# Kernel tuning notes

Measured on AMD Instinct MI355X. Metric: run time of the kernel, lower is better.

The kernel has to match this reference:

```python
import jax, jax.numpy as jnp
import numpy as np

B, C, LO, LQ, H = 64, 4, 64, 128, 768
NEG = -10000.0


def _trilinear(u, um, v, vm, w1, b1, w2, b2, w3):
    # u: [N, Lu, H], v: [N, Lv, H]; returns [N, Lu, Lv]
    p1 = u @ w1 + b1                                  # [N, Lu, 1]
    p2 = (v @ w2 + b2).transpose(0, 2, 1)             # [N, 1, Lv]
    p3 = jnp.einsum('bud,bvd->buv', u * w3, v)        # trilinear term
    return p1 + p2 + p3 + ((1.0 - um) * NEG)[:, :, None] + ((1.0 - vm) * NEG)[:, None, :]


def _forward(encoded_o, encoded_q, om, qm,
             att_W1_w, att_W1_b, att_W2_w, att_W2_b, att_W3,
             Wc_self_w, Wc_self_b, Wc_w, Wc_b, Va_w, Va_b, Wg_w, Wg_b,
             co_W1_w, co_W1_b, co_W2_w, co_W2_b, co_W3, Wp_w, Wp_b,
             sa_W1_w, sa_W1_b, sa_W2_w, sa_W2_b, sa_W3, Wf_w, Wf_b):
    b, c, lo, h = encoded_o.shape
    lq = encoded_q.shape[2]
    p = c * (c - 1)
    # ---- pairwise option-compare (OCN_Att_layer) over all (i, j), j != i ----
    i_idx = np.repeat(np.arange(c), c - 1)
    j_idx = np.array([j for i in range(c) for j in range(c) if j != i])
    o_i = encoded_o[:, i_idx].reshape(b * p, lo, h)   # 'ok'
    o_j = encoded_o[:, j_idx].reshape(b * p, lo, h)   # 'ol'
    m_i = om[:, i_idx].reshape(b * p, lo)
    m_j = om[:, j_idx].reshape(b * p, lo)
    A = _trilinear(o_j, m_j, o_i, m_i, att_W1_w, att_W1_b, att_W2_w, att_W2_b, att_W3)
    att = jax.nn.softmax(A, axis=1)
    olk_ctx = jnp.einsum('bud,buv->bvd', o_j, att)    # [BP, LO, H]
    OLK = jnp.concatenate([o_i - olk_ctx, o_i * olk_ctx], axis=-1)  # [BP, LO, 2H]
    cmp_proj = OLK @ Wc_w + Wc_b                      # Wc applied per compare pair
    cmp_sum = cmp_proj.reshape(b, c, c - 1, lo, h).sum(axis=2).reshape(b * c, lo, h)
    # ---- merge layer (per candidate, flattened into batch) ----
    o1 = encoded_o.reshape(b * c, lo, h)
    q = encoded_q.reshape(b * c, lq, h)
    omf = om.reshape(b * c, lo)
    qmf = qm.reshape(b * c, lq)
    Aq = jax.nn.softmax(q @ Va_w + Va_b + ((1.0 - qmf) * NEG)[:, :, None], axis=1)  # [BC, LQ, 1]
    Q = jnp.einsum('bld,blo->bod', q, Aq)             # [BC, 1, H]
    OCK = jnp.tanh(o1 @ Wc_self_w + Wc_self_b + cmp_sum)
    Qb = jnp.broadcast_to(Q, (b * c, lo, h))
    G = jax.nn.sigmoid(jnp.concatenate([o1, OCK, Qb], axis=-1) @ Wg_w + Wg_b)
    merged = G * o1 + (1.0 - G) * OCK                 # [BC, LO, H]
    # ---- co-attention with question ----
    A2 = _trilinear(q, qmf, merged, omf, co_W1_w, co_W1_b, co_W2_w, co_W2_b, co_W3)  # [BC, LQ, LO]
    ACK = jax.nn.softmax(A2, axis=2)
    OA = jnp.einsum('bqo,bod->bqd', ACK, merged)      # [BC, LQ, H]
    APK = jax.nn.softmax(A2, axis=1)
    dOA = jnp.concatenate([q, OA], axis=-1)           # [BC, LQ, 2H]
    POAA = jnp.einsum('bqd,bqo->bod', dOA, APK)       # [BC, LO, 2H]
    OPK = jax.nn.relu(jnp.concatenate([merged, POAA], axis=-1) @ Wp_w + Wp_b)
    # ---- self-attention ----
    A3 = _trilinear(OPK, omf, OPK, omf, sa_W1_w, sa_W1_b, sa_W2_w, sa_W2_b, sa_W3)
    att3 = jax.nn.softmax(A3, axis=1)
    OSK = jnp.einsum('bud,buv->bvd', OPK, att3)
    OFK = jax.nn.relu(jnp.concatenate([OPK, OSK, OPK - OSK, OPK * OSK], axis=-1) @ Wf_w + Wf_b)
    return OFK.reshape(b, c, lo, h).max(axis=2)       # [B, C, H]


def setup_inputs():
    ks = jax.random.split(jax.random.key(0), 32)
    def p(i, shape, s=0.02):
        return jax.random.normal(ks[i], shape, jnp.float32) * s
    return {
        'encoded_o': jax.random.normal(ks[0], (B, C, LO, H), jnp.float32),
        'encoded_q': jax.random.normal(ks[1], (B, C, LQ, H), jnp.float32),
        'option_mask': jnp.ones((B, C, LO), jnp.int32),
        'question_mask': jnp.ones((B, C, LQ), jnp.int32),
        'att_W1_w': p(2, (H, 1)), 'att_W1_b': p(3, (1,)),
        'att_W2_w': p(4, (H, 1)), 'att_W2_b': p(5, (1,)),
        'att_W3': p(6, (H,)),
        'Wc_self_w': p(7, (H, H)), 'Wc_self_b': p(8, (H,)),
        'Wc_w': p(9, (2 * H, H)), 'Wc_b': p(10, (H,)),
        'Va_w': p(11, (H, 1)), 'Va_b': p(12, (1,)),
        'Wg_w': p(13, (3 * H, H)), 'Wg_b': p(14, (H,)),
        'co_W1_w': p(15, (H, 1)), 'co_W1_b': p(16, (1,)),
        'co_W2_w': p(17, (H, 1)), 'co_W2_b': p(18, (1,)),
        'co_W3': p(19, (H,)),
        'Wp_w': p(20, (3 * H, H)), 'Wp_b': p(21, (H,)),
        'sa_W1_w': p(22, (H, 1)), 'sa_W1_b': p(23, (1,)),
        'sa_W2_w': p(24, (H, 1)), 'sa_W2_b': p(25, (1,)),
        'sa_W3': p(26, (H,)),
        'Wf_w': p(27, (4 * H, H)), 'Wf_b': p(28, (H,)),
    }


def reference(encoded_o, encoded_q, option_mask, question_mask,
              att_W1_w, att_W1_b, att_W2_w, att_W2_b, att_W3,
              Wc_self_w, Wc_self_b, Wc_w, Wc_b, Va_w, Va_b, Wg_w, Wg_b,
              co_W1_w, co_W1_b, co_W2_w, co_W2_b, co_W3, Wp_w, Wp_b,
              sa_W1_w, sa_W1_b, sa_W2_w, sa_W2_b, sa_W3, Wf_w, Wf_b):
    return _forward(encoded_o, encoded_q,
                    option_mask.astype(jnp.float32), question_mask.astype(jnp.float32),
                    att_W1_w, att_W1_b, att_W2_w, att_W2_b, att_W3,
                    Wc_self_w, Wc_self_b, Wc_w, Wc_b, Va_w, Va_b, Wg_w, Wg_b,
                    co_W1_w, co_W1_b, co_W2_w, co_W2_b, co_W3, Wp_w, Wp_b,
                    sa_W1_w, sa_W1_b, sa_W2_w, sa_W2_b, sa_W3, Wf_w, Wf_b)
```

## Files before the change

kernel.cpp:

```cpp
#include <hip/hip_runtime.h>
#include <math.h>


#define NEGC (-10000.0f)
constexpr int HD = 768;
constexpr int KSTR = 9216;

constexpr int EP_TANH = 1;
constexpr int EP_MERGE = 2;
constexpr int EP_RELU = 3;
constexpr int EP_RELU_MAX = 4;

typedef __attribute__((ext_vector_type(8))) short bf16x8;
typedef __attribute__((ext_vector_type(8))) unsigned short u16x8;
typedef __attribute__((ext_vector_type(4))) unsigned short u16x4;
typedef __attribute__((ext_vector_type(4))) float f32x4;

__device__ inline void st8(float* dst, float4 a0, float4 a1) {
  dst[0] = a0.x; dst[1] = a0.y; dst[2] = a0.z; dst[3] = a0.w;
  dst[4] = a1.x; dst[5] = a1.y; dst[6] = a1.z; dst[7] = a1.w;
}

__device__ inline unsigned short f2bf(float x) {
  unsigned int u = __float_as_uint(x);
  u += 0x7fffu + ((u >> 16) & 1u);
  return (unsigned short)(u >> 16);
}

__device__ inline float bf2f(unsigned short u) {
  return __uint_as_float(((unsigned int)u) << 16);
}

__device__ inline u16x8 pack8(float4 a, float4 b) {
  u16x8 r;
  r[0] = f2bf(a.x); r[1] = f2bf(a.y); r[2] = f2bf(a.z); r[3] = f2bf(a.w);
  r[4] = f2bf(b.x); r[5] = f2bf(b.y); r[6] = f2bf(b.z); r[7] = f2bf(b.w);
  return r;
}

__device__ inline u16x4 pack4(float4 a) {
  u16x4 r;
  r[0] = f2bf(a.x); r[1] = f2bf(a.y); r[2] = f2bf(a.z); r[3] = f2bf(a.w);
  return r;
}

__device__ inline void gload_lds16(const unsigned short* src, unsigned short* dst) {
  __builtin_amdgcn_global_load_lds(
      (const __attribute__((address_space(1))) void*)src,
      (__attribute__((address_space(3))) void*)dst, 16, 0, 0);
}

__global__ __launch_bounds__(256)
void bfprep_dot_kernel(const float* __restrict__ x, const float* __restrict__ w3,
                       const float* __restrict__ w1, const float* __restrict__ b1,
                       const float* __restrict__ w2, const float* __restrict__ b2,
                       unsigned short* __restrict__ xbf, unsigned short* __restrict__ xw3,
                       float* __restrict__ o1, float* __restrict__ o2, int ntok) {
  int tok = blockIdx.x * 4 + (threadIdx.x >> 6);
  int lane = threadIdx.x & 63;
  if (tok >= ntok) return;
  const float* xp = x + (size_t)tok * HD;
  unsigned short* xb = xbf + (size_t)tok * HD;
  unsigned short* xw = xw3 + (size_t)tok * HD;
  float s1 = 0.f, s2 = 0.f;
#pragma unroll
  for (int i = 0; i < 3; ++i) {
    int c = (lane + (i << 6)) << 2;
    float4 xv = *(const float4*)(xp + c);
    float4 w3v = *(const float4*)(w3 + c);
    float4 wa = *(const float4*)(w1 + c);
    float4 wb = *(const float4*)(w2 + c);
    s1 = fmaf(xv.x, wa.x, s1); s1 = fmaf(xv.y, wa.y, s1);
    s1 = fmaf(xv.z, wa.z, s1); s1 = fmaf(xv.w, wa.w, s1);
    s2 = fmaf(xv.x, wb.x, s2); s2 = fmaf(xv.y, wb.y, s2);
    s2 = fmaf(xv.z, wb.z, s2); s2 = fmaf(xv.w, wb.w, s2);
    *(u16x4*)(xb + c) = pack4(xv);
    float4 sv;
    sv.x = xv.x * w3v.x; sv.y = xv.y * w3v.y; sv.z = xv.z * w3v.z; sv.w = xv.w * w3v.w;
    *(u16x4*)(xw + c) = pack4(sv);
  }
#pragma unroll
  for (int off = 32; off; off >>= 1) {
    s1 += __shfl_xor(s1, off);
    s2 += __shfl_xor(s2, off);
  }
  if (lane == 0) { o1[tok] = s1 + b1[0]; o2[tok] = s2 + b2[0]; }
}

__global__ __launch_bounds__(256)
void opkprep_kernel(const unsigned short* __restrict__ x, const float* __restrict__ w3,
                    const float* __restrict__ w1, const float* __restrict__ b1,
                    const float* __restrict__ w2, const float* __restrict__ b2,
                    unsigned short* __restrict__ xw3,
                    float* __restrict__ o1, float* __restrict__ o2, int ntok) {
  int tok = blockIdx.x * 4 + (threadIdx.x >> 6);
  int lane = threadIdx.x & 63;
  if (tok >= ntok) return;
  const unsigned short* xp = x + (size_t)tok * HD;
  unsigned short* xw = xw3 + (size_t)tok * HD;
  float s1 = 0.f, s2 = 0.f;
#pragma unroll
  for (int i = 0; i < 3; ++i) {
    int c = (lane + (i << 6)) << 2;
    u16x4 xv = *(const u16x4*)(xp + c);
    float x0 = bf2f(xv[0]), x1 = bf2f(xv[1]), x2 = bf2f(xv[2]), x3 = bf2f(xv[3]);
    float4 w3v = *(const float4*)(w3 + c);
    float4 wa = *(const float4*)(w1 + c);
    float4 wb = *(const float4*)(w2 + c);
    s1 = fmaf(x0, wa.x, s1); s1 = fmaf(x1, wa.y, s1);
    s1 = fmaf(x2, wa.z, s1); s1 = fmaf(x3, wa.w, s1);
    s2 = fmaf(x0, wb.x, s2); s2 = fmaf(x1, wb.y, s2);
    s2 = fmaf(x2, wb.z, s2); s2 = fmaf(x3, wb.w, s2);
    u16x4 sv;
    sv[0] = f2bf(x0 * w3v.x); sv[1] = f2bf(x1 * w3v.y);
    sv[2] = f2bf(x2 * w3v.z); sv[3] = f2bf(x3 * w3v.w);
    *(u16x4*)(xw + c) = sv;
  }
#pragma unroll
  for (int off = 32; off; off >>= 1) {
    s1 += __shfl_xor(s1, off);
    s2 += __shfl_xor(s2, off);
  }
  if (lane == 0) { o1[tok] = s1 + b1[0]; o2[tok] = s2 + b2[0]; }
}

__global__ __launch_bounds__(256)
void qpool2_kernel(const float* __restrict__ q,
                   const float* __restrict__ Va_w, const float* __restrict__ Va_b,
                   const float* __restrict__ coW1_w, const float* __restrict__ coW1_b,
                   const int* __restrict__ qm,
                   float* __restrict__ qco1, float* __restrict__ Q) {
  __shared__ float qa_s[128];
  __shared__ float wgt[128];
  __shared__ float wred[4];
  const int t = threadIdx.x, bc = blockIdx.x;
  const int lane = t & 63, wv = t >> 6;
  const float* qb = q + (size_t)bc * (128 * HD);
  for (int it = 0; it < 32; ++it) {
    const int tl = it * 4 + wv;
    const float* xp = qb + (size_t)tl * HD;
    float s1 = 0.f, s2 = 0.f;
#pragma unroll
    for (int i = 0; i < 3; ++i) {
      int c = (lane + (i << 6)) << 2;
      float4 xv = *(const float4*)(xp + c);
      float4 wa = *(const float4*)(Va_w + c);
      float4 wb = *(const float4*)(coW1_w + c);
      s1 = fmaf(xv.x, wa.x, s1); s1 = fmaf(xv.y, wa.y, s1);
      s1 = fmaf(xv.z, wa.z, s1); s1 = fmaf(xv.w, wa.w, s1);
      s2 = fmaf(xv.x, wb.x, s2); s2 = fmaf(xv.y, wb.y, s2);
      s2 = fmaf(xv.z, wb.z, s2); s2 = fmaf(xv.w, wb.w, s2);
    }
#pragma unroll
    for (int off = 32; off; off >>= 1) {
      s1 += __shfl_xor(s1, off);
      s2 += __shfl_xor(s2, off);
    }
    if (lane == 0) {
      qa_s[tl] = s1 + Va_b[0];
      qco1[bc * 128 + tl] = s2 + coW1_b[0];
    }
  }
  __syncthreads();
  const int* qmp = qm + bc * 128;
  float v = -1e30f;
  if (t < 128) v = qa_s[t] + (1.f - (float)qmp[t]) * NEGC;
  float m = v;
#pragma unroll
  for (int off = 32; off; off >>= 1) m = fmaxf(m, __shfl_xor(m, off));
  if ((t & 63) == 0) wred[t >> 6] = m;
  __syncthreads();
  float gm = fmaxf(fmaxf(wred[0], wred[1]), fmaxf(wred[2], wred[3]));
  float e = (t < 128) ? expf(v - gm) : 0.f;
  float s = e;
#pragma unroll
  for (int off = 32; off; off >>= 1) s += __shfl_xor(s, off);
  __syncthreads();
  if ((t & 63) == 0) wred[t >> 6] = s;
  __syncthreads();
  float tot = wred[0] + wred[1] + wred[2] + wred[3];
  if (t < 128) wgt[t] = e / tot;
  __syncthreads();
  float* Qp = Q + (size_t)bc * HD;
  for (int d = t; d < HD; d += 256) {
    float acc = 0.f;
    for (int l = 0; l < 128; ++l) acc = fmaf(wgt[l], qb[(size_t)l * HD + d], acc);
    Qp[d] = acc;
  }
}

template<int NJ>
__global__ __launch_bounds__(256)
void p1_kernel(const unsigned short* __restrict__ Xbf, const unsigned short* __restrict__ Xw3,
               const float* __restrict__ s1g, const float* __restrict__ s2g,
               const int* __restrict__ maskg, unsigned short* __restrict__ PtG) {
  __shared__ __align__(16) unsigned short Ua[64 * 136];
  __shared__ __align__(16) unsigned short Vb[64 * 136];
  __shared__ float Sbuf[64][66];
  __shared__ float red[4][64];
  const int t = threadIdx.x;
  int ubc, vbc;
  if (NJ == 1) {
    ubc = vbc = blockIdx.x;
  } else {
    const int b = blockIdx.x / 12, pr = blockIdx.x % 12;
    const int i = pr / 3, jj = pr % 3;
    const int j = jj + (jj >= i ? 1 : 0);
    vbc = (b << 2) + i; ubc = (b << 2) + j;
  }
  const unsigned short* U = Xbf + (size_t)ubc * (64 * HD);
  const unsigned short* V = Xw3 + (size_t)vbc * (64 * HD);
  const int w = t >> 6, lane = t & 63, l15 = lane & 15, l4 = lane >> 4;
  const int srow = t >> 2, scol = (t & 3) << 5;
  f32x4 acc[4] = {};
  for (int k0 = 0; k0 < HD; k0 += 128) {
    const unsigned short* up = U + (size_t)srow * HD + k0 + scol;
    const unsigned short* vp = V + (size_t)srow * HD + k0 + scol;
    unsigned short* ua = &Ua[srow * 136 + scol];
    unsigned short* vb = &Vb[srow * 136 + scol];
#pragma unroll
    for (int z = 0; z < 4; ++z) {
      *(u16x8*)(ua + z * 8) = *(const u16x8*)(up + z * 8);
      *(u16x8*)(vb + z * 8) = *(const u16x8*)(vp + z * 8);
    }
    __syncthreads();
#pragma unroll
    for (int ks = 0; ks < 4; ++ks) {
      bf16x8 af = *(const bf16x8*)(&Ua[(w * 16 + l15) * 136 + ks * 32 + l4 * 8]);
#pragma unroll
      for (int n = 0; n < 4; ++n) {
        bf16x8 bf = *(const bf16x8*)(&Vb[(n * 16 + l15) * 136 + ks * 32 + l4 * 8]);
        acc[n] = __builtin_amdgcn_mfma_f32_16x16x32_bf16(af, bf, acc[n], 0, 0, 0);
      }
    }
    __syncthreads();
  }
  {
    float s1v[4];
#pragma unroll
    for (int r = 0; r < 4; ++r) {
      int u = w * 16 + l4 * 4 + r;
      s1v[r] = s1g[ubc * 64 + u] + (1.f - (float)maskg[ubc * 64 + u]) * NEGC;
    }
#pragma unroll
    for (int n = 0; n < 4; ++n) {
      int v = n * 16 + l15;
      float s2v = s2g[vbc * 64 + v] + (1.f - (float)maskg[vbc * 64 + v]) * NEGC;
#pragma unroll
      for (int r = 0; r < 4; ++r)
        Sbuf[w * 16 + l4 * 4 + r][v] = acc[n][r] + s1v[r] + s2v;
    }
  }
  __syncthreads();
  {
    const int v = t & 63, part = t >> 6;
    float m = -1e30f;
#pragma unroll
    for (int z = 0; z < 16; ++z) m = fmaxf(m, Sbuf[part * 16 + z][v]);
    red[part][v] = m;
    __syncthreads();
    float gm = fmaxf(fmaxf(red[0][v], red[1][v]), fmaxf(red[2][v], red[3][v]));
    float s = 0.f;
#pragma unroll
    for (int z = 0; z < 16; ++z) {
      float e = expf(Sbuf[part * 16 + z][v] - gm);
      Sbuf[part * 16 + z][v] = e;
      s += e;
    }
    __syncthreads();
    red[part][v] = s;
    __syncthreads();
    float cinv = 1.f / (red[0][v] + red[1][v] + red[2][v] + red[3][v]);
    unsigned short* pt = PtG + (size_t)blockIdx.x * 4096 + v * 64 + part * 16;
#pragma unroll
    for (int z = 0; z < 16; ++z) pt[z] = f2bf(Sbuf[part * 16 + z][v] * cinv);
  }
}

template<int NJ>
__global__ __launch_bounds__(256)
void p2_kernel(const unsigned short* __restrict__ Xbf, const unsigned short* __restrict__ PtG,
               const unsigned short* __restrict__ Oi,
               unsigned short* __restrict__ osk,
               unsigned short* __restrict__ y1, unsigned short* __restrict__ y2) {
  __shared__ __align__(16) unsigned short Pts[NJ][64 * 72];
  __shared__ __align__(16) unsigned short U2[64 * 192];
  const int t = threadIdx.x;
  const int dq = blockIdx.x, bc = blockIdx.y;
  const int d0 = dq * 192;
  const int b = bc >> 2, i = bc & 3;
  const int w = t >> 6, lane = t & 63, l15 = lane & 15, l4 = lane >> 4;
  {
    const int v = t >> 2, cs = (t & 3) << 4;
#pragma unroll
    for (int jj = 0; jj < NJ; ++jj) {
      size_t src = (NJ == 1 ? (size_t)bc : (size_t)(b * 12 + i * 3 + jj)) * 4096 + v * 64 + cs;
      *(u16x8*)(&Pts[jj][v * 72 + cs]) = *(const u16x8*)(PtG + src);
      *(u16x8*)(&Pts[jj][v * 72 + cs + 8]) = *(const u16x8*)(PtG + src + 8);
    }
  }
  f32x4 acc[4][3] = {};
  const int su = t >> 2, sc0 = (t & 3) * 48;
  const int sswz = ((su >> 3) & 3) << 5;
  for (int jj = 0; jj < NJ; ++jj) {
    const int ubc = (NJ == 1) ? bc : ((b << 2) + (jj + (jj >= i ? 1 : 0)));
    __syncthreads();
    {
      const unsigned short* up = Xbf + (size_t)ubc * (64 * HD) + (size_t)su * HD + d0 + sc0;
#pragma unroll
      for (int it = 0; it < 6; ++it) {
        u16x8 vdat = *(const u16x8*)(up + it * 8);
        *(u16x8*)((char*)U2 + ((su * 384 + (sc0 + it * 8) * 2) ^ sswz)) = vdat;
      }
    }
    __syncthreads();
    const unsigned short* ptj = &Pts[jj][0];
#pragma unroll
    for (int ks = 0; ks < 2; ++ks) {
      bf16x8 bfr[3];
#pragma unroll
      for (int n = 0; n < 3; ++n) {
        const int col = (w * 3 + n) * 16 + l15;
#pragma unroll
        for (int e = 0; e < 8; ++e) {
          const int uk = ks * 32 + l4 * 8 + e;
          const int byte = (uk * 384 + col * 2) ^ (((uk >> 3) & 3) << 5);
          bfr[n][e] = *(const short*)((const char*)U2 + byte);
        }
      }
#pragma unroll
      for (int m = 0; m < 4; ++m) {
        bf16x8 af = *(const bf16x8*)(ptj + (m * 16 + l15) * 72 + ks * 32 + l4 * 8);
#pragma unroll
        for (int n = 0; n < 3; ++n)
          acc[m][n] = __builtin_amdgcn_mfma_f32_16x16x32_bf16(af, bfr[n], acc[m][n], 0, 0, 0);
      }
    }
  }
  const unsigned short* oip = Oi + (size_t)bc * (64 * HD);
  const size_t obase = (size_t)bc * (64 * HD);
#pragma unroll
  for (int m = 0; m < 4; ++m)
#pragma unroll
    for (int n = 0; n < 3; ++n) {
      const int d = d0 + (w * 3 + n) * 16 + l15;
#pragma unroll
      for (int r = 0; r < 4; ++r) {
        const int v = m * 16 + l4 * 4 + r;
        const size_t idx = obase + (size_t)v * HD + d;
        const float cs = acc[m][n][r];
        const float oi = bf2f(oip[(size_t)v * HD + d]);
        if (NJ == 3) {
          y1[idx] = f2bf(fmaf(3.f, oi, -cs));
          y2[idx] = f2bf(oi * cs);
        } else {
          osk[idx] = f2bf(cs);
          y1[idx] = f2bf(oi - cs);
          y2[idx] = f2bf(oi * cs);
        }
      }
    }
}

__global__ __launch_bounds__(256)
void poaa2_kernel(const float* __restrict__ qin, const unsigned short* __restrict__ mergedb,
                  const float* __restrict__ qco1,
                  const float* __restrict__ coW2_w, const float* __restrict__ coW2_b,
                  const int* __restrict__ qm, const int* __restrict__ om,
                  const float* __restrict__ w3,
                  unsigned short* __restrict__ PLO, unsigned short* __restrict__ PHI) {
  __shared__ __align__(16) char smem[77312];
  __shared__ float red[4][64];
  __shared__ float rowm[128], rowfac[128];
  __shared__ float colfac[64];
  __shared__ float ms2_s[64];
  __shared__ float gmax_s;
  float* T = (float*)smem;
  unsigned short* Aq = (unsigned short*)smem;
  unsigned short* Bm = (unsigned short*)(smem + 18432);
  unsigned short* Tt = (unsigned short*)(smem + 33280);
  unsigned short* Tft = (unsigned short*)(smem + 50688);
  unsigned short* M2bf = (unsigned short*)(smem + 68096);
  unsigned short* Qc = (unsigned short*)smem;
  unsigned short* Mc = (unsigned short*)(smem + 18432);

  const int t = threadIdx.x, dqh = blockIdx.x, bc = blockIdx.y;
  const int w = t >> 6, lane = t & 63, l15 = lane & 15, l4 = lane >> 4;
  const float* qp = qin + (size_t)bc * (128 * HD);
  const unsigned short* mp = mergedb + (size_t)bc * (64 * HD);
  const float* qc = qco1 + bc * 128;
  const int* qmp = qm + bc * 128;
  const int* omp = om + bc * 64;

  {
    const int arow = t >> 1, acs = (t & 1) << 5;
    const int brow = t >> 2, bcs = (t & 3) << 4;
    f32x4 acc[2][4] = {};
    float msacc = 0.f;
    for (int k0 = 0; k0 < HD; k0 += 64) {
      {
        const float* p = qp + (size_t)arow * HD + k0 + acs;
        const float* wp = w3 + k0 + acs;
        unsigned short* dst = &Aq[arow * 72 + acs];
#pragma unroll
        for (int z = 0; z < 4; ++z) {
          float4 a = *(const float4*)(p + z * 8);
          float4 b = *(const float4*)(p + z * 8 + 4);
          float4 wa = *(const float4*)(wp + z * 8);
          float4 wb = *(const float4*)(wp + z * 8 + 4);
          a.x *= wa.x; a.y *= wa.y; a.z *= wa.z; a.w *= wa.w;
          b.x *= wb.x; b.y *= wb.y; b.z *= wb.z; b.w *= wb.w;
          *(u16x8*)(dst + z * 8) = pack8(a, b);
        }
      }
      {
        const unsigned short* p = mp + (size_t)brow * HD + k0 + bcs;
        unsigned short* dst = &Bm[brow * 72 + bcs];
        u16x8 v0 = *(const u16x8*)(p);
        u16x8 v1 = *(const u16x8*)(p + 8);
        *(u16x8*)(dst) = v0;
        *(u16x8*)(dst + 8) = v1;
        const float* wp = coW2_w + k0 + bcs;
        float4 wa = *(const float4*)(wp);
        float4 wb = *(const float4*)(wp + 4);
        float4 wc = *(const float4*)(wp + 8);
        float4 wd = *(const float4*)(wp + 12);
        msacc = fmaf(bf2f(v0[0]), wa.x, msacc); msacc = fmaf(bf2f(v0[1]), wa.y, msacc);
        msacc = fmaf(bf2f(v0[2]), wa.z, msacc); msacc = fmaf(bf2f(v0[3]), wa.w, msacc);
        msacc = fmaf(bf2f(v0[4]), wb.x, msacc); msacc = fmaf(bf2f(v0[5]), wb.y, msacc);
        msacc = fmaf(bf2f(v0[6]), wb.z, msacc); msacc = fmaf(bf2f(v0[7]), wb.w, msacc);
        msacc = fmaf(bf2f(v1[0]), wc.x, msacc); msacc = fmaf(bf2f(v1[1]), wc.y, msacc);
        msacc = fmaf(bf2f(v1[2]), wc.z, msacc); msacc = fmaf(bf2f(v1[3]), wc.w, msacc);
        msacc = fmaf(bf2f(v1[4]), wd.x, msacc); msacc = fmaf(bf2f(v1[5]), wd.y, msacc);
        msacc = fmaf(bf2f(v1[6]), wd.z, msacc); msacc = fmaf(bf2f(v1[7]), wd.w, msacc);
      }
      __syncthreads();
#pragma unroll
      for (int ks = 0; ks < 2; ++ks) {
        bf16x8 af[2], bf[4];
#pragma unroll
        for (int m = 0; m < 2; ++m)
          af[m] = *(const bf16x8*)(&Aq[(w * 32 + m * 16 + l15) * 72 + ks * 32 + l4 * 8]);
#pragma unroll
        for (int n = 0; n < 4; ++n)
          bf[n] = *(const bf16x8*)(&Bm[(n * 16 + l15) * 72 + ks * 32 + l4 * 8]);
#pragma unroll
        for (int m = 0; m < 2; ++m)
#pragma unroll
          for (int n = 0; n < 4; ++n)
            acc[m][n] = __builtin_amdgcn_mfma_f32_16x16x32_bf16(af[m], bf[n], acc[m][n], 0, 0, 0);
      }
      __syncthreads();
    }
    msacc += __shfl_xor(msacc, 1);
    msacc += __shfl_xor(msacc, 2);
    if ((t & 3) == 0) ms2_s[brow] = msacc + coW2_b[0];
    __syncthreads();
#pragma unroll
    for (int n = 0; n < 4; ++n) {
      const int v = n * 16 + l15;
      const float ct = ms2_s[v] + (1.f - (float)omp[v]) * NEGC;
#pragma unroll
      for (int m = 0; m < 2; ++m)
#pragma unroll
        for (int r = 0; r < 4; ++r) {
          const int qrow = w * 32 + m * 16 + l4 * 4 + r;
          const float rt = qc[qrow] + (1.f - (float)qmp[qrow]) * NEGC;
          T[qrow * 65 + v] = acc[m][n][r] + rt + ct;
        }
    }
  }
  __syncthreads();
  {
    int qrow = t >> 1, h = t & 1;
    float m = -1e30f;
    for (int v = h * 32; v < h * 32 + 32; ++v) m = fmaxf(m, T[qrow * 65 + v]);
    m = fmaxf(m, __shfl_xor(m, 1));
    float s = 0.f;
    for (int v = h * 32; v < h * 32 + 32; ++v) s += expf(T[qrow * 65 + v] - m);
    s += __shfl_xor(s, 1);
    if (h == 0) { rowm[qrow] = m; rowfac[qrow] = s; }
  }
  float colm_loc = 0.f;
  {
    int v = t & 63, part = t >> 6;
    float m = -1e30f;
    for (int qq = part * 32; qq < part * 32 + 32; ++qq) m = fmaxf(m, T[qq * 65 + v]);
    red[part][v] = m;
    __syncthreads();
    float cm = fmaxf(fmaxf(red[0][v], red[1][v]), fmaxf(red[2][v], red[3][v]));
    float s = 0.f;
    for (int qq = part * 32; qq < part * 32 + 32; ++qq) s += expf(T[qq * 65 + v] - cm);
    __syncthreads();
    red[part][v] = s;
    __syncthreads();
    if (part == 0) { colm_loc = cm; colfac[v] = red[0][v] + red[1][v] + red[2][v] + red[3][v]; }
  }
  __syncthreads();
  if (t < 64) {
    float m = fmaxf(rowm[t], rowm[t + 64]);
#pragma unroll
    for (int off = 32; off; off >>= 1) m = fmaxf(m, __shfl_xor(m, off));
    if (t == 0) gmax_s = m;
  }
  __syncthreads();
  const float gmax = gmax_s;
  if (t < 128) rowfac[t] = expf(fminf(gmax - rowm[t], 60.f)) / rowfac[t];
  if (t < 64) colfac[t] = expf(fminf(gmax - colm_loc, 60.f)) / colfac[t];
  __syncthreads();
  {
    const int o = t >> 2, qs = (t & 3) << 5;
    for (int z = 0; z < 32; ++z) {
      const int qq = qs + z;
      float e = expf(T[qq * 65 + o] - gmax);
      Tt[o * 136 + qq] = f2bf(e);
      Tft[o * 136 + qq] = f2bf(e * rowfac[qq]);
    }
  }
  __syncthreads();
  {
    f32x4 m2acc[4] = {};
#pragma unroll
    for (int ks = 0; ks < 4; ++ks) {
      bf16x8 af = *(const bf16x8*)(&Tt[(w * 16 + l15) * 136 + ks * 32 + l4 * 8]);
#pragma unroll
      for (int n = 0; n < 4; ++n) {
        bf16x8 bf = *(const bf16x8*)(&Tft[(n * 16 + l15) * 136 + ks * 32 + l4 * 8]);
        m2acc[n] = __builtin_amdgcn_mfma_f32_16x16x32_bf16(af, bf, m2acc[n], 0, 0, 0);
      }
    }
#pragma unroll
    for (int n = 0; n < 4; ++n)
#pragma unroll
      for (int r = 0; r < 4; ++r) {
        const int o = w * 16 + l4 * 4 + r;
        M2bf[o * 72 + n * 16 + l15] = f2bf(colfac[o] * m2acc[n][r]);
      }
  }
  const int dql = t >> 1, dqs = (t & 1) << 5;
  const int dml = t >> 2, dms = (t & 3) << 4;
  const int swq = ((dql >> 3) & 3) << 5;
  const int swm = ((dml >> 3) & 3) << 5;
  unsigned short* plo = PLO + (size_t)bc * (64 * HD);
  unsigned short* phi = PHI + (size_t)bc * (64 * HD);
  for (int dc = dqh * 6; dc < dqh * 6 + 6; ++dc) {
    const int d0 = dc * 64;
    __syncthreads();
    {
      const float* p = qp + (size_t)dql * HD + d0 + dqs;
#pragma unroll
      for (int z = 0; z < 4; ++z) {
        float4 a = *(const float4*)(p + z * 8);
        float4 b = *(const float4*)(p + z * 8 + 4);
        *(u16x8*)((char*)Qc + ((dql * 144 + (dqs + z * 8) * 2) ^ swq)) = pack8(a, b);
      }
    }
    {
      const unsigned short* p = mp + (size_t)dml * HD + d0 + dms;
      *(u16x8*)((char*)Mc + ((dml * 144 + dms * 2) ^ swm)) = *(const u16x8*)p;
      *(u16x8*)((char*)Mc + ((dml * 144 + (dms + 8) * 2) ^ swm)) = *(const u16x8*)(p + 8);
    }
    __syncthreads();
    const int col = w * 16 + l15;
    f32x4 lacc[4] = {};
#pragma unroll
    for (int ks = 0; ks < 4; ++ks) {
      bf16x8 bf;
#pragma unroll
      for (int e = 0; e < 8; ++e) {
        const int qq = ks * 32 + l4 * 8 + e;
        bf[e] = *(const short*)((const char*)Qc + ((qq * 144 + col * 2) ^ (((qq >> 3) & 3) << 5)));
      }
#pragma unroll
      for (int m = 0; m < 4; ++m) {
        bf16x8 af = *(const bf16x8*)(&Tt[(m * 16 + l15) * 136 + ks * 32 + l4 * 8]);
        lacc[m] = __builtin_amdgcn_mfma_f32_16x16x32_bf16(af, bf, lacc[m], 0, 0, 0);
      }
    }
    f32x4 pacc[4] = {};
#pragma unroll
    for (int ks = 0; ks < 2; ++ks) {
      bf16x8 bf;
#pragma unroll
      for (int e = 0; e < 8; ++e) {
        const int vv = ks * 32 + l4 * 8 + e;
        bf[e] = *(const short*)((const char*)Mc + ((vv * 144 + col * 2) ^ (((vv >> 3) & 3) << 5)));
      }
#pragma unroll
      for (int m = 0; m < 4; ++m) {
        bf16x8 af = *(const bf16x8*)(&M2bf[(m * 16 + l15) * 72 + ks * 32 + l4 * 8]);
        pacc[m] = __builtin_amdgcn_mfma_f32_16x16x32_bf16(af, bf, pacc[m], 0, 0, 0);
      }
    }
#pragma unroll
    for (int m = 0; m < 4; ++m)
#pragma unroll
      for (int r = 0; r < 4; ++r) {
        const int o = m * 16 + l4 * 4 + r;
        const int d = d0 + w * 16 + l15;
        plo[(size_t)o * HD + d] = f2bf(colfac[o] * lacc[m][r]);
        phi[(size_t)o * HD + d] = f2bf(pacc[m][r]);
      }
  }
}

struct GemmArgs {
  const float* a[4];
  const float* w[4];
  int nchunks;
  const float* bias;
  float* out;
};

__global__ __launch_bounds__(256)
void gemm_store_kernel(GemmArgs g) {
  __shared__ float As[64][33];
  __shared__ float Ws[32][65];
  const int t = threadIdx.x;
  const int m0 = blockIdx.y << 6, n0 = blockIdx.x << 6;
  const int tr = t >> 4, tc = t & 15;
  float acc[4][4];
#pragma unroll
  for (int x = 0; x < 4; ++x)
#pragma unroll
    for (int y = 0; y < 4; ++y) acc[x][y] = 0.f;
  const int arow = t >> 2, acs = (t & 3) << 3;
  const int wrow = t >> 3, wcs = (t & 7) << 3;
  for (int c = 0; c < g.nchunks; ++c) {
    const float* Ap = g.a[c] + (size_t)(m0 + arow) * HD + acs;
    const float* Wp = g.w[c] + (size_t)wrow * HD + n0 + wcs;
    for (int k0 = 0; k0 < HD; k0 += 32) {
      float4 a0 = *(const float4*)(Ap + k0);
      float4 a1 = *(const float4*)(Ap + k0 + 4);
      st8(&As[arow][acs], a0, a1);
      float4 w0 = *(const float4*)(Wp + (size_t)k0 * HD);
      float4 w1 = *(const float4*)(Wp + (size_t)k0 * HD + 4);
      st8(&Ws[wrow][wcs], w0, w1);
      __syncthreads();
#pragma unroll
      for (int kk = 0; kk < 32; ++kk) {
        float av[4], bv[4];
#pragma unroll
        for (int x = 0; x < 4; ++x) av[x] = As[(tr << 2) + x][kk];
#pragma unroll
        for (int y = 0; y < 4; ++y) bv[y] = Ws[kk][(tc << 2) + y];
#pragma unroll
        for (int x = 0; x < 4; ++x)
#pragma unroll
          for (int y = 0; y < 4; ++y) acc[x][y] = fmaf(av[x], bv[y], acc[x][y]);
      }
      __syncthreads();
    }
  }
#pragma unroll
  for (int x = 0; x < 4; ++x) {
    const int r = m0 + (tr << 2) + x;
#pragma unroll
    for (int y = 0; y < 4; ++y) {
      const int n = n0 + (tc << 2) + y;
      g.out[(size_t)r * HD + n] = acc[x][y] + g.bias[n];
    }
  }
}

struct WcAllArgs {
  const float* src[12];
  int basecol[12];
  unsigned short* dst;
};

__global__ __launch_bounds__(256)
void wconv_all_kernel(WcAllArgs g) {
  __shared__ float tile[64][65];
  const int slice = blockIdx.y;
  const float* src = g.src[slice];
  const int bi = blockIdx.x % 12, bj = blockIdx.x / 12;
  const int t = threadIdx.x;
  const int r = t >> 2, cseg = (t & 3) << 4;
  const float* p = src + (size_t)(bi * 64 + r) * HD + bj * 64 + cseg;
#pragma unroll
  for (int j = 0; j < 16; j += 4) {
    float4 v = *(const float4*)(p + j);
    tile[r][cseg + j + 0] = v.x; tile[r][cseg + j + 1] = v.y;
    tile[r][cseg + j + 2] = v.z; tile[r][cseg + j + 3] = v.w;
  }
  __syncthreads();
  unsigned short* q = g.dst + (size_t)(bj * 64 + r) * KSTR + g.basecol[slice] + bi * 64 + cseg;
  u16x8 lo, hi;
#pragma unroll
  for (int j = 0; j < 8; ++j) lo[j] = f2bf(tile[cseg + j][r]);
#pragma unroll
  for (int j = 0; j < 8; ++j) hi[j] = f2bf(tile[cseg + 8 + j][r]);
  *(u16x8*)q = lo;
  *(u16x8*)(q + 8) = hi;
}

struct MMArgs {
  const unsigned short* a[4];
  int K;
  const unsigned short* wt;
  const float* bias;
  const float* bias2;
  const unsigned short* aux0;
  const unsigned short* aux1;
  const float* aux2;
  float* outf;
  unsigned short* outb;
};

template<int EP>
__global__ __launch_bounds__(512)
void mfma_gemm_kernel(MMArgs g) {
  __shared__ __align__(16) unsigned short As[3][128 * 32];
  __shared__ __align__(16) unsigned short Bs[3][128 * 32];
  const int t = threadIdx.x;
  const int lane = t & 63, w = t >> 6;
  const int wr = w >> 2, wc = w & 3;
  const int m0 = blockIdx.x << 7, n0 = blockIdx.y << 7;
  const int l15 = lane & 15, l4 = lane >> 4;
  f32x4 acc[4][2] = {};

  const int srow = w * 16 + (lane >> 2);
  const int gcol = (((lane & 3) ^ ((lane >> 3) & 3))) * 8;
  const int rsw = (l15 >> 1) & 3;
  const int rcol = ((l4 ^ rsw)) * 8;

  const int nkt = g.K >> 5;

  auto issue = [&](int kt, int buf) {
    const int c = kt / 24;
    const int koff = (kt - c * 24) << 5;
    const unsigned short* ap = g.a[c] + (size_t)(m0 + srow) * HD + koff + gcol;
    const unsigned short* bp = g.wt + (size_t)(n0 + srow) * KSTR + (kt << 5) + gcol;
    gload_lds16(ap, &As[buf][w * 512]);
    gload_lds16(bp, &Bs[buf][w * 512]);
  };

  auto compute = [&](int kt, int buf, bool prefetch) {
    bf16x8 af[4], bfr[2];
#pragma unroll
    for (int mi = 0; mi < 4; ++mi)
      af[mi] = *(const bf16x8*)(&As[buf][(wr * 64 + mi * 16 + l15) * 32 + rcol]);
#pragma unroll
    for (int ni = 0; ni < 2; ++ni)
      bfr[ni] = *(const bf16x8*)(&Bs[buf][(wc * 32 + ni * 16 + l15) * 32 + rcol]);
    asm volatile("s_waitcnt lgkmcnt(0)" ::: "memory");
    __builtin_amdgcn_s_barrier();
    if (prefetch) issue(kt + 3, buf);
    __builtin_amdgcn_s_setprio(1);
#pragma unroll
    for (int mi = 0; mi < 4; ++mi)
#pragma unroll
      for (int ni = 0; ni < 2; ++ni)
        acc[mi][ni] = __builtin_amdgcn_mfma_f32_16x16x32_bf16(af[mi], bfr[ni], acc[mi][ni], 0, 0, 0);
    __builtin_amdgcn_s_setprio(0);
  };

  issue(0, 0); issue(1, 1); issue(2, 2);
  int buf = 0;
  int kt = 0;
  for (; kt < nkt - 2; ++kt) {
    asm volatile("s_waitcnt vmcnt(4)" ::: "memory");
    __builtin_amdgcn_s_barrier();
    compute(kt, buf, kt + 3 < nkt);
    buf = (buf == 2) ? 0 : buf + 1;
  }
  asm volatile("s_waitcnt vmcnt(2)" ::: "memory");
  __builtin_amdgcn_s_barrier();
  compute(kt, buf, false);
  buf = (buf == 2) ? 0 : buf + 1;
  ++kt;
  asm volatile("s_waitcnt vmcnt(0)" ::: "memory");
  __builtin_amdgcn_s_barrier();
  compute(kt, buf, false);

  if (EP == EP_RELU_MAX) {
#pragma unroll
    for (int ni = 0; ni < 2; ++ni) {
      const int n = n0 + wc * 32 + ni * 16 + l15;
      const float b = g.bias[n];
      float m = 0.f;
#pragma unroll
      for (int mi = 0; mi < 4; ++mi)
#pragma unroll
        for (int r = 0; r < 4; ++r)
          m = fmaxf(m, acc[mi][ni][r] + b);
      m = fmaxf(m, 0.f);
      m = fmaxf(m, __shfl_xor(m, 16));
      m = fmaxf(m, __shfl_xor(m, 32));
      if (l4 == 0) g.outf[(size_t)((m0 >> 6) + wr) * HD + n] = m;
    }
  } else {
#pragma unroll
    for (int mi = 0; mi < 4; ++mi)
#pragma unroll
      for (int r = 0; r < 4; ++r) {
        const int row = m0 + wr * 64 + mi * 16 + l4 * 4 + r;
#pragma unroll
        for (int ni = 0; ni < 2; ++ni) {
          const int n = n0 + wc * 32 + ni * 16 + l15;
          const size_t oi = (size_t)row * HD + n;
          float v = acc[mi][ni][r];
          if (EP == EP_TANH) {
            g.outb[oi] = f2bf(tanhf(v + g.bias[n] + 3.f * g.bias2[n]));
          } else if (EP == EP_MERGE) {
            float gg = v + g.aux2[(size_t)(row >> 6) * HD + n];
            float sg = 1.f / (1.f + expf(-gg));
            float o1v = bf2f(g.aux0[oi]);
            float ock = bf2f(g.aux1[oi]);
            g.outb[oi] = f2bf(fmaf(sg, o1v - ock, ock));
          } else {
            g.outb[oi] = f2bf(fmaxf(v + g.bias[n], 0.f));
          }
        }
      }
  }
}

extern "C" void kernel_launch(void* const* d_in, const int* in_sizes, int n_in,
                              void* d_out, int out_size, void* d_ws, size_t ws_size,
                              hipStream_t stream) {
  const float* enc_o = (const float*)d_in[0];
  const float* enc_q = (const float*)d_in[1];
  const int* om = (const int*)d_in[2];
  const int* qm = (const int*)d_in[3];
  const float* att_W1_w = (const float*)d_in[4];
  const float* att_W1_b = (const float*)d_in[5];
  const float* att_W2_w = (const float*)d_in[6];
  const float* att_W2_b = (const float*)d_in[7];
  const float* att_W3 = (const float*)d_in[8];
  const float* Wc_self_w = (const float*)d_in[9];
  const float* Wc_self_b = (const float*)d_in[10];
  const float* Wc_w = (const float*)d_in[11];
  const float* Wc_b = (const float*)d_in[12];
  const float* Va_w = (const float*)d_in[13];
  const float* Va_b = (const float*)d_in[14];
  const float* Wg_w = (const float*)d_in[15];
  const float* Wg_b = (const float*)d_in[16];
  const float* co_W1_w = (const float*)d_in[17];
  const float* co_W1_b = (const float*)d_in[18];
  const float* co_W2_w = (const float*)d_in[19];
  const float* co_W2_b = (const float*)d_in[20];
  const float* co_W3 = (const float*)d_in[21];
  const float* Wp_w = (const float*)d_in[22];
  const float* Wp_b = (const float*)d_in[23];
  const float* sa_W1_w = (const float*)d_in[24];
  const float* sa_W1_b = (const float*)d_in[25];
  const float* sa_W2_w = (const float*)d_in[26];
  const float* sa_W2_b = (const float*)d_in[27];
  const float* sa_W3 = (const float*)d_in[28];
  const float* Wf_w = (const float*)d_in[29];
  const float* Wf_b = (const float*)d_in[30];
  float* out = (float*)d_out;

  const int NTOK_O = 16384;
  const int HH = 768 * 768;

  float* ws = (float*)d_ws;
  size_t off = 0;
  auto carve = [&](size_t n) { float* p = ws + off; off += n; return p; };
  float* s1o   = carve(16384);
  float* s2o   = carve(16384);
  float* qco1  = carve(32768);
  float* sa1   = carve(16384);
  float* sa2   = carve(16384);
  float* Qpool = carve(196608);
  float* Qg    = carve(196608);
  float* A2buf = carve(2097152);
  float* r1 = carve(12582912);
  float* r2 = carve(12582912);
  float* r3 = carve(12582912);
  float* r4 = carve(12582912);
  if (ws_size < off * sizeof(float)) return;
  unsigned short* OPKb  = (unsigned short*)r1;
  unsigned short* X1    = (unsigned short*)(r1 + 6291456);
  unsigned short* X3    = (unsigned short*)(r1 + 6291456);
  unsigned short* OCKb  = (unsigned short*)r2;
  unsigned short* PLOb  = (unsigned short*)r2;
  unsigned short* opkw3 = (unsigned short*)r2;
  unsigned short* X2    = (unsigned short*)(r2 + 6291456);
  unsigned short* MRGb  = (unsigned short*)r3;
  unsigned short* OSKb  = (unsigned short*)r3;
  unsigned short* X4    = (unsigned short*)(r3 + 6291456);
  unsigned short* eobf  = (unsigned short*)r4;
  unsigned short* eow3  = (unsigned short*)(r4 + 6291456);
  unsigned short* PHIb  = (unsigned short*)r4;
  unsigned short* wall  = (unsigned short*)(r4 + 6291456);
  unsigned short* PtG   = (unsigned short*)A2buf;

  const dim3 GBIG(128, 6);

  bfprep_dot_kernel<<<NTOK_O / 4, 256, 0, stream>>>(enc_o, att_W3, att_W1_w, att_W1_b,
                                                    att_W2_w, att_W2_b, eobf, eow3,
                                                    s1o, s2o, NTOK_O);
  qpool2_kernel<<<256, 256, 0, stream>>>(enc_q, Va_w, Va_b, co_W1_w, co_W1_b,
                                         qm, qco1, Qpool);

  p1_kernel<3><<<768, 256, 0, stream>>>(eobf, eow3, s1o, s2o, om, PtG);
  {
    WcAllArgs wa{};
    wa.src[0] = Wc_self_w; wa.src[1] = Wc_w;        wa.src[2] = Wc_w + HH;
    wa.src[3] = Wg_w;      wa.src[4] = Wg_w + HH;
    wa.src[5] = Wp_w;      wa.src[6] = Wp_w + HH;   wa.src[7] = Wp_w + 2 * HH;
    wa.src[8] = Wf_w;      wa.src[9] = Wf_w + HH;   wa.src[10] = Wf_w + 2 * HH;
    wa.src[11] = Wf_w + 3 * HH;
    int bases[12] = {0, 768, 1536, 2304, 3072, 3840, 4608, 5376, 6144, 6912, 7680, 8448};
    for (int i = 0; i < 12; ++i) wa.basecol[i] = bases[i];
    wa.dst = wall;
    wconv_all_kernel<<<dim3(144, 12), 256, 0, stream>>>(wa);
  }
  p2_kernel<3><<<dim3(4, 256), 256, 0, stream>>>(eobf, PtG, eobf, nullptr, X1, X2);

  {
    MMArgs g{};
    g.a[0] = eobf; g.a[1] = X1; g.a[2] = X2;
    g.K = 2304; g.wt = wall + 0;
    g.bias = Wc_self_b; g.bias2 = Wc_b; g.outb = OCKb;
    mfma_gemm_kernel<EP_TANH><<<GBIG, 512, 0, stream>>>(g);
  }

  {
    GemmArgs g{};
    g.a[0] = Qpool; g.w[0] = Wg_w + 2 * HH;
    g.nchunks = 1; g.bias = Wg_b; g.out = Qg;
    gemm_store_kernel<<<dim3(12, 4), 256, 0, stream>>>(g);
  }

  {
    MMArgs g{};
    g.a[0] = eobf; g.a[1] = OCKb;
    g.K = 1536; g.wt = wall + 2304; g.bias = nullptr;
    g.aux0 = eobf; g.aux1 = OCKb; g.aux2 = Qg; g.outb = MRGb;
    mfma_gemm_kernel<EP_MERGE><<<GBIG, 512, 0, stream>>>(g);
  }

  poaa2_kernel<<<dim3(2, 256), 256, 0, stream>>>(enc_q, MRGb, qco1, co_W2_w, co_W2_b,
                                                 qm, om, co_W3, PLOb, PHIb);

  {
    MMArgs g{};
    g.a[0] = MRGb; g.a[1] = PLOb; g.a[2] = PHIb;
    g.K = 2304; g.wt = wall + 3840; g.bias = Wp_b; g.outb = OPKb;
    mfma_gemm_kernel<EP_RELU><<<GBIG, 512, 0, stream>>>(g);
  }

  opkprep_kernel<<<NTOK_O / 4, 256, 0, stream>>>(OPKb, sa_W3, sa_W1_w, sa_W1_b,
                                                 sa_W2_w, sa_W2_b, opkw3, sa1, sa2, NTOK_O);
  p1_kernel<1><<<256, 256, 0, stream>>>(OPKb, opkw3, sa1, sa2, om, PtG);
  p2_kernel<1><<<dim3(4, 256), 256, 0, stream>>>(OPKb, PtG, OPKb, OSKb, X3, X4);

  {
    MMArgs g{};
    g.a[0] = OPKb; g.a[1] = OSKb; g.a[2] = X3; g.a[3] = X4;
    g.K = 3072; g.wt = wall + 6144; g.bias = Wf_b; g.outf = out;
    mfma_gemm_kernel<EP_RELU_MAX><<<GBIG, 512, 0, stream>>>(g);
  }
}
```

Baseline: 599.6 us.

## Widen GEMM K-tile to 64 with double buffering instead of triple buffering

The MFMA GEMM now stages 64-wide K slices (two loads per wave per operand) into two LDS buffers instead of 32-wide slices into three. It uses a new XOR swizzle over 8 segments for the 64-wide rows. This halves the number of K iterations and barriers and gives more MFMAs per barrier. In exchange it reduces prefetch depth from three stages to two, and LDS use rises from 48KB to 64KB, which could lower occupancy.

```diff
diff --git a/kernel.cpp b/kernel.cpp
--- a/kernel.cpp
+++ b/kernel.cpp
@@ -711,8 +711,8 @@
 template<int EP>
 __global__ __launch_bounds__(512)
 void mfma_gemm_kernel(MMArgs g) {
-  __shared__ __align__(16) unsigned short As[3][128 * 32];
-  __shared__ __align__(16) unsigned short Bs[3][128 * 32];
+  __shared__ __align__(16) unsigned short As[2][128 * 64];
+  __shared__ __align__(16) unsigned short Bs[2][128 * 64];
   const int t = threadIdx.x;
   const int lane = t & 63, w = t >> 6;
   const int wr = w >> 2, wc = w & 3;
@@ -720,59 +720,65 @@
   const int l15 = lane & 15, l4 = lane >> 4;
   f32x4 acc[4][2] = {};
 
-  const int srow = w * 16 + (lane >> 2);
-  const int gcol = (((lane & 3) ^ ((lane >> 3) & 3))) * 8;
-  const int rsw = (l15 >> 1) & 3;
-  const int rcol = ((l4 ^ rsw)) * 8;
-
-  const int nkt = g.K >> 5;
+  const int gseg = ((lane & 7) ^ ((lane >> 3) & 7)) * 8;
+  const int irow = lane >> 3;
+
+  const int nkt = g.K >> 6;
 
   auto issue = [&](int kt, int buf) {
-    const int c = kt / 24;
-    const int koff = (kt - c * 24) << 5;
-    const unsigned short* ap = g.a[c] + (size_t)(m0 + srow) * HD + koff + gcol;
-    const unsigned short* bp = g.wt + (size_t)(n0 + srow) * KSTR + (kt << 5) + gcol;
-    gload_lds16(ap, &As[buf][w * 512]);
-    gload_lds16(bp, &Bs[buf][w * 512]);
+    const int c = kt / 12;
+    const int koff = (kt - c * 12) << 6;
+#pragma unroll
+    for (int i = 0; i < 2; ++i) {
+      const int grow = w * 16 + i * 8 + irow;
+      const unsigned short* ap = g.a[c] + (size_t)(m0 + grow) * HD + koff + gseg;
+      const unsigned short* bp = g.wt + (size_t)(n0 + grow) * KSTR + (kt << 6) + gseg;
+      gload_lds16(ap, &As[buf][w * 1024 + i * 512]);
+      gload_lds16(bp, &Bs[buf][w * 1024 + i * 512]);
+    }
   };
 
   auto compute = [&](int kt, int buf, bool prefetch) {
-    bf16x8 af[4], bfr[2];
-#pragma unroll
-    for (int mi = 0; mi < 4; ++mi)
-      af[mi] = *(const bf16x8*)(&As[buf][(wr * 64 + mi * 16 + l15) * 32 + rcol]);
-#pragma unroll
-    for (int ni = 0; ni < 2; ++ni)
-      bfr[ni] = *(const bf16x8*)(&Bs[buf][(wc * 32 + ni * 16 + l15) * 32 + rcol]);
+    bf16x8 af[2][4], bfr[2][2];
+#pragma unroll
+    for (int kk = 0; kk < 2; ++kk) {
+#pragma unroll
+      for (int mi = 0; mi < 4; ++mi) {
+        const int row = wr * 64 + mi * 16 + l15;
+        const int seg = (kk * 4 + l4) ^ (l15 & 7);
+        af[kk][mi] = *(const bf16x8*)(&As[buf][row * 64 + seg * 8]);
+      }
+#pragma unroll
+      for (int ni = 0; ni < 2; ++ni) {
+        const int row = wc * 32 + ni * 16 + l15;
+        const int seg = (kk * 4 + l4) ^ (l15 & 7);
+        bfr[kk][ni] = *(const bf16x8*)(&Bs[buf][row * 64 + seg * 8]);
+      }
+    }
     asm volatile("s_waitcnt lgkmcnt(0)" ::: "memory");
     __builtin_amdgcn_s_barrier();
-    if (prefetch) issue(kt + 3, buf);
+    if (prefetch) issue(kt + 2, buf);
     __builtin_amdgcn_s_setprio(1);
 #pragma unroll
-    for (int mi = 0; mi < 4; ++mi)
-#pragma unroll
-      for (int ni = 0; ni < 2; ++ni)
-        acc[mi][ni] = __builtin_amdgcn_mfma_f32_16x16x32_bf16(af[mi], bfr[ni], acc[mi][ni], 0, 0, 0);
+    for (int kk = 0; kk < 2; ++kk)
+#pragma unroll
+      for (int mi = 0; mi < 4; ++mi)
+#pragma unroll
+        for (int ni = 0; ni < 2; ++ni)
+          acc[mi][ni] = __builtin_amdgcn_mfma_f32_16x16x32_bf16(af[kk][mi], bfr[kk][ni], acc[mi][ni], 0, 0, 0);
     __builtin_amdgcn_s_setprio(0);
   };
 
-  issue(0, 0); issue(1, 1); issue(2, 2);
-  int buf = 0;
+  issue(0, 0); issue(1, 1);
   int kt = 0;
-  for (; kt < nkt - 2; ++kt) {
+  for (; kt < nkt - 1; ++kt) {
     asm volatile("s_waitcnt vmcnt(4)" ::: "memory");
     __builtin_amdgcn_s_barrier();
-    compute(kt, buf, kt + 3 < nkt);
-    buf = (buf == 2) ? 0 : buf + 1;
-  }
-  asm volatile("s_waitcnt vmcnt(2)" ::: "memory");
-  __builtin_amdgcn_s_barrier();
-  compute(kt, buf, false);
-  buf = (buf == 2) ? 0 : buf + 1;
-  ++kt;
+    compute(kt, kt & 1, kt + 2 < nkt);
+  }
   asm volatile("s_waitcnt vmcnt(0)" ::: "memory");
   __builtin_amdgcn_s_barrier();
-  compute(kt, buf, false);
+  compute(kt, kt & 1, false);
 
   if (EP == EP_RELU_MAX) {
 #pragma unroll
```

Measured after the change: 626.6 us. +4.5%, slower.
